# Performance work log

Measured on AMD Instinct MI355X. Metric: run time of the kernel, lower is better.

## Reference

```python
import jax, jax.numpy as jnp
import numpy as np

K = 12
CHUNK = 1024
N_LAYERS = 4
WIDTH = 192
COND = 64
PE_DIM = 3 * 8 * 2 + 3  # 51
OUT_SCALE = 0.01
BIG = 1e9


def _build_knn(x, k=K, chunk=CHUNK):
    """Brute-force kNN, row-chunked like the TF double-chunked version.
    x: (N,3) float32 -> (N,k) int32 neighbor indices (self excluded)."""
    n = x.shape[0]
    x = x.astype(jnp.float32)
    x_sq = jnp.sum(x * x, axis=1)  # (N,)
    col_ids = jnp.arange(n, dtype=jnp.int32)
    starts = jnp.arange(0, n, chunk, dtype=jnp.int32)

    def one_chunk(start):
        xc = jax.lax.dynamic_slice(x, (start, 0), (chunk, 3))        # (chunk,3)
        sq_c = jax.lax.dynamic_slice(x_sq, (start,), (chunk,))       # (chunk,)
        d = sq_c[:, None] + x_sq[None, :] - 2.0 * (xc @ x.T)         # (chunk,N)
        d = jnp.maximum(d, 0.0)
        rows = start + jnp.arange(chunk, dtype=jnp.int32)
        d = d + jnp.where(rows[:, None] == col_ids[None, :], BIG, 0.0)  # exclude self
        _, idx = jax.lax.top_k(-d, k)                                 # smallest distances
        return idx.astype(jnp.int32)

    idx = jax.lax.map(one_chunk, starts)  # (n/chunk, chunk, k)
    return idx.reshape(n, k)


def _fourier(x, Bs):
    """concat_k [sin(xB_k), cos(xB_k)] + x  -> (N, PE_DIM)."""
    feats = []
    for B in Bs:
        xb = x @ B  # (N,8)
        feats.append(jnp.sin(xb))
        feats.append(jnp.cos(xb))
    feats.append(x)
    return jnp.concatenate(feats, axis=-1)


def setup_inputs() -> dict:
    key = jax.random.key(0)
    ks = jax.random.split(key, 16)
    n = 32768
    x = jax.random.normal(ks[0], (n, 3), dtype=jnp.float32)
    z = jax.random.normal(ks[1], (COND,), dtype=jnp.float32)
    sigmas = (1.0, 10.0, 50.0)
    B0 = jax.random.normal(ks[2], (3, 8), dtype=jnp.float32) * sigmas[0]
    B1 = jax.random.normal(ks[3], (3, 8), dtype=jnp.float32) * sigmas[1]
    B2 = jax.random.normal(ks[4], (3, 8), dtype=jnp.float32) * sigmas[2]
    in_total = PE_DIM + COND  # 115
    s = 0.05
    Wp = jax.random.normal(ks[5], (in_total, WIDTH), dtype=jnp.float32) * s
    bp = jnp.zeros((WIDTH,), dtype=jnp.float32)
    mix_dim = WIDTH + WIDTH + 6  # feat + agg + rel_feat
    Wl = jax.random.normal(ks[6], (N_LAYERS, mix_dim, WIDTH), dtype=jnp.float32) * s
    bl = jnp.zeros((N_LAYERS, WIDTH), dtype=jnp.float32)
    # FiLM: kernel ~zeros, gamma bias=ones, beta bias=zeros (perturbed slightly)
    Wg = jax.random.normal(ks[7], (N_LAYERS, COND, WIDTH), dtype=jnp.float32) * 0.01
    bg = jnp.ones((N_LAYERS, WIDTH), dtype=jnp.float32)
    Wb = jax.random.normal(ks[8], (N_LAYERS, COND, WIDTH), dtype=jnp.float32) * 0.01
    bb = jnp.zeros((N_LAYERS, WIDTH), dtype=jnp.float32)
    Wout = jax.random.normal(ks[9], (WIDTH, 3), dtype=jnp.float32) * s
    bout = jnp.zeros((3,), dtype=jnp.float32)
    return {"x": x, "z": z, "B0": B0, "B1": B1, "B2": B2,
            "Wp": Wp, "bp": bp, "Wl": Wl, "bl": bl,
            "Wg": Wg, "bg": bg, "Wb": Wb, "bb": bb,
            "Wout": Wout, "bout": bout}


def reference(x, z, B0, B1, B2, Wp, bp, Wl, bl, Wg, bg, Wb, bb, Wout, bout):
    n = x.shape[0]
    knn_idx = _build_knn(x)                     # (N,K) int32
    pe = _fourier(x, (B0, B1, B2))              # (N,51)
    zb = jnp.broadcast_to(z[None, :], (n, COND))
    feat = jnp.concatenate([pe, zb], axis=-1)   # (N,115)
    h = jax.nn.silu(feat @ Wp + bp)             # (N,WIDTH)
    # precompute relative-coordinate stats (same for all layers)
    nbr_coords = x[knn_idx]                     # (N,K,3)
    rel = nbr_coords - x[:, None, :]
    rel_feat = jnp.concatenate([rel.mean(axis=1), rel.std(axis=1)], axis=-1)  # (N,6)
    for li in range(N_LAYERS):
        nbr = h[knn_idx]                        # (N,K,WIDTH) gather
        agg = nbr.mean(axis=1)                  # (N,WIDTH)
        mix = jnp.concatenate([h, agg, rel_feat], axis=-1)  # (N,390)
        h = jax.nn.silu(mix @ Wl[li] + bl[li])
        gamma = z @ Wg[li] + bg[li]             # (WIDTH,)
        beta = z @ Wb[li] + bb[li]
        h = h * gamma[None, :] + beta[None, :]  # FiLM
    out = (h @ Wout + bout) * OUT_SCALE         # (N,3)
    return out
```

## Files before the change

kernel.cpp:

```cpp
#include <hip/hip_runtime.h>
#include <math.h>

#define WIDTH 192
#define KNN 12
#define G 64
#define NCELLS (G * G * G)
#define SMAX 8

#define CE(a, b) { double _lo = fmin(a, b); double _hi = fmax(a, b); a = _lo; b = _hi; }
#define INSERT12(key) { \
    b11 = fmin(b11, key); \
    CE(b10, b11); CE(b9, b10); CE(b8, b9); CE(b7, b8); CE(b6, b7); \
    CE(b5, b6);  CE(b4, b5); CE(b3, b4); CE(b2, b3); CE(b1, b2); CE(b0, b1); }
#define DECL12 double b0,b1,b2,b3,b4,b5,b6,b7,b8,b9,b10,b11
#define INIT12 { b0=__hiloint2double(0x7F7FFFFF,0);  b1=__hiloint2double(0x7F7FFFFF,1); \
    b2=__hiloint2double(0x7F7FFFFF,2);  b3=__hiloint2double(0x7F7FFFFF,3); \
    b4=__hiloint2double(0x7F7FFFFF,4);  b5=__hiloint2double(0x7F7FFFFF,5); \
    b6=__hiloint2double(0x7F7FFFFF,6);  b7=__hiloint2double(0x7F7FFFFF,7); \
    b8=__hiloint2double(0x7F7FFFFF,8);  b9=__hiloint2double(0x7F7FFFFF,9); \
    b10=__hiloint2double(0x7F7FFFFF,10); b11=__hiloint2double(0x7F7FFFFF,11); }

#define MERGE_STAGE(m) { \
    double pb11 = shflx_d(b11, m), pb10 = shflx_d(b10, m), pb9 = shflx_d(b9, m); \
    double pb8  = shflx_d(b8, m),  pb7  = shflx_d(b7, m),  pb6 = shflx_d(b6, m); \
    double pb5  = shflx_d(b5, m),  pb4  = shflx_d(b4, m),  pb3 = shflx_d(b3, m); \
    double pb2  = shflx_d(b2, m),  pb1  = shflx_d(b1, m),  pb0 = shflx_d(b0, m); \
    double c12 = pb3, c13 = pb2, c14 = pb1, c15 = pb0; \
    b4 = fmin(b4, pb11); b5 = fmin(b5, pb10); b6 = fmin(b6, pb9);  b7 = fmin(b7, pb8); \
    b8 = fmin(b8, pb7);  b9 = fmin(b9, pb6);  b10 = fmin(b10, pb5); b11 = fmin(b11, pb4); \
    CE(b0, b8);  CE(b1, b9);  CE(b2, b10); CE(b3, b11); \
    CE(b4, c12); CE(b5, c13); CE(b6, c14); CE(b7, c15); \
    CE(b0, b4);  CE(b1, b5);  CE(b2, b6);  CE(b3, b7); \
    CE(b8, c12); CE(b9, c13); CE(b10, c14); CE(b11, c15); \
    CE(b0, b2);  CE(b1, b3);  CE(b4, b6);  CE(b5, b7); \
    CE(b8, b10); CE(b9, b11); \
    CE(b0, b1);  CE(b2, b3);  CE(b4, b5);  CE(b6, b7); \
    CE(b8, b9);  CE(b10, b11); }

__device__ inline unsigned encf(float f) {
    unsigned u = __float_as_uint(f);
    return (u & 0x80000000u) ? ~u : (u | 0x80000000u);
}
__device__ inline float decf(unsigned u) {
    return (u & 0x80000000u) ? __uint_as_float(u & 0x7fffffffu) : __uint_as_float(~u);
}
__device__ inline int cellc(float v, float mn, float invh) {
    int c = (int)((v - mn) * invh);
    return min(max(c, 0), G - 1);
}
__device__ inline double shflx_d(double v, int m) {
    int lo = __shfl_xor(__double2loint(v), m, 64);
    int hi = __shfl_xor(__double2hiint(v), m, 64);
    return __hiloint2double(hi, lo);
}

__global__ __launch_bounds__(256) void prep_kernel(
    const float4* __restrict__ sorted, const float* __restrict__ B0,
    const float* __restrict__ B1, const float* __restrict__ B2,
    float* __restrict__ pe, int n)
{
    int i = blockIdx.x * 256 + threadIdx.x;
    float4 q = sorted[i];
    float x0 = q.x, x1 = q.y, x2 = q.z;
    const float* Bm[3] = {B0, B1, B2};
    float* pr = pe + (size_t)i * 64;
#pragma unroll
    for (int m = 0; m < 3; ++m) {
        const float* B = Bm[m];
#pragma unroll
        for (int k = 0; k < 8; ++k) {
            float arg = x0 * B[k] + x1 * B[8 + k] + x2 * B[16 + k];
            pr[m * 16 + k]     = sinf(arg);
            pr[m * 16 + 8 + k] = cosf(arg);
        }
    }
    pr[48] = x0; pr[49] = x1; pr[50] = x2;
#pragma unroll
    for (int c = 51; c < 64; ++c) pr[c] = 0.0f;
}

__global__ __launch_bounds__(256) void precompute_kernel(
    const float* __restrict__ z, const float* __restrict__ Wp, const float* __restrict__ bp,
    const float* __restrict__ Wg, const float* __restrict__ bg,
    const float* __restrict__ Wb, const float* __restrict__ bb,
    float* __restrict__ bias0, float* __restrict__ gammaB, float* __restrict__ betaB)
{
    __shared__ float zs[64];
    int t = threadIdx.x;
    if (t < 64) zs[t] = z[t];
    __syncthreads();
    if (t < WIDTH) {
        float acc = bp[t];
        for (int k = 0; k < 64; ++k) acc += zs[k] * Wp[(51 + k) * WIDTH + t];
        bias0[t] = acc;
        for (int l = 0; l < 4; ++l) {
            float g = bg[l * WIDTH + t];
            float b = bb[l * WIDTH + t];
            for (int k = 0; k < 64; ++k) {
                g += zs[k] * Wg[(l * 64 + k) * WIDTH + t];
                b += zs[k] * Wb[(l * 64 + k) * WIDTH + t];
            }
            gammaB[l * WIDTH + t] = g;
            betaB[l * WIDTH + t] = b;
        }
    }
}

__global__ __launch_bounds__(64) void init_bbox_kernel(unsigned* __restrict__ bb)
{
    int t = threadIdx.x;
    if (t < 3) bb[t] = 0xFFFFFFFFu;
    else if (t < 6) bb[t] = 0u;
}

__global__ __launch_bounds__(256) void bbox_kernel(
    const float* __restrict__ x, unsigned* __restrict__ bb, int n)
{
    int i = blockIdx.x * 256 + threadIdx.x;
    unsigned emin[3], emax[3];
#pragma unroll
    for (int a = 0; a < 3; ++a) { unsigned e = encf(x[i * 3 + a]); emin[a] = e; emax[a] = e; }
#pragma unroll
    for (int o = 32; o; o >>= 1) {
#pragma unroll
        for (int a = 0; a < 3; ++a) {
            emin[a] = min(emin[a], (unsigned)__shfl_xor((int)emin[a], o, 64));
            emax[a] = max(emax[a], (unsigned)__shfl_xor((int)emax[a], o, 64));
        }
    }
    if ((threadIdx.x & 63) == 0) {
#pragma unroll
        for (int a = 0; a < 3; ++a) {
            atomicMin(&bb[a], emin[a]);
            atomicMax(&bb[3 + a], emax[a]);
        }
    }
}

__global__ __launch_bounds__(256) void hist_kernel(
    const float* __restrict__ x, const unsigned* __restrict__ bb,
    unsigned* __restrict__ counts, unsigned long long* __restrict__ rowmask, int n)
{
    int i = blockIdx.x * 256 + threadIdx.x;
    float mnx = decf(bb[0]), mny = decf(bb[1]), mnz = decf(bb[2]);
    float ivx = (float)G / (decf(bb[3]) - mnx);
    float ivy = (float)G / (decf(bb[4]) - mny);
    float ivz = (float)G / (decf(bb[5]) - mnz);
    int cx = cellc(x[i * 3 + 0], mnx, ivx);
    int cy = cellc(x[i * 3 + 1], mny, ivy);
    int cz = cellc(x[i * 3 + 2], mnz, ivz);
    atomicAdd(&counts[(cz * G + cy) * G + cx], 1u);
    atomicOr(&rowmask[cz * G + cy], 1ull << cx);
}

__global__ __launch_bounds__(256) void scan1_kernel(
    const unsigned* __restrict__ counts, unsigned* __restrict__ offs,
    unsigned* __restrict__ bsums)
{
    __shared__ unsigned s[256];
    int b = blockIdx.x, t = threadIdx.x;
    unsigned base = (unsigned)b * 1024 + t * 4;
    unsigned v[4], sum = 0;
#pragma unroll
    for (int k = 0; k < 4; ++k) { v[k] = counts[base + k]; sum += v[k]; }
    s[t] = sum; __syncthreads();
    for (int off = 1; off < 256; off <<= 1) {
        unsigned xv = (t >= off) ? s[t - off] : 0u;
        __syncthreads();
        s[t] += xv;
        __syncthreads();
    }
    unsigned excl = s[t] - sum;
    if (t == 255) bsums[b] = s[255];
    unsigned run = excl;
#pragma unroll
    for (int k = 0; k < 4; ++k) { offs[base + k] = run; run += v[k]; }
}

__global__ __launch_bounds__(256) void scan2_kernel(unsigned* __restrict__ bsums)
{
    __shared__ unsigned s[256];
    int t = threadIdx.x;
    unsigned v = bsums[t];
    s[t] = v; __syncthreads();
    for (int off = 1; off < 256; off <<= 1) {
        unsigned xv = (t >= off) ? s[t - off] : 0u;
        __syncthreads();
        s[t] += xv;
        __syncthreads();
    }
    bsums[t] = s[t] - v;
}

__global__ __launch_bounds__(256) void scan3_kernel(
    unsigned* __restrict__ offs, const unsigned* __restrict__ bsums,
    unsigned* __restrict__ cursors, int n)
{
    int b = blockIdx.x, t = threadIdx.x;
    unsigned add = bsums[b];
    unsigned base = (unsigned)b * 1024 + t * 4;
#pragma unroll
    for (int k = 0; k < 4; ++k) {
        unsigned v = offs[base + k] + add;
        offs[base + k] = v;
        cursors[base + k] = v;
    }
    if (b == 255 && t == 255) offs[NCELLS] = (unsigned)n;
}

__global__ __launch_bounds__(256) void scatter_kernel(
    const float* __restrict__ x, const unsigned* __restrict__ bb,
    unsigned* __restrict__ cursors, float4* __restrict__ sorted,
    unsigned* __restrict__ inv, int n)
{
    int i = blockIdx.x * 256 + threadIdx.x;
    float mnx = decf(bb[0]), mny = decf(bb[1]), mnz = decf(bb[2]);
    float ivx = (float)G / (decf(bb[3]) - mnx);
    float ivy = (float)G / (decf(bb[4]) - mny);
    float ivz = (float)G / (decf(bb[5]) - mnz);
    float x0 = x[i * 3 + 0], x1 = x[i * 3 + 1], x2 = x[i * 3 + 2];
    int cx = cellc(x0, mnx, ivx);
    int cy = cellc(x1, mny, ivy);
    int cz = cellc(x2, mnz, ivz);
    unsigned pos = atomicAdd(&cursors[(cz * G + cy) * G + cx], 1u);
    sorted[pos] = make_float4(x0, x1, x2, __int_as_float(i));
    inv[i] = pos;
}

__global__ __launch_bounds__(64) void knn_grid_kernel(
    const float4* __restrict__ sorted, const unsigned* __restrict__ offs,
    const unsigned long long* __restrict__ rowmask,
    const unsigned* __restrict__ bb, const float* __restrict__ x,
    const unsigned* __restrict__ inv,
    unsigned short* __restrict__ knn, float* __restrict__ relf, int n)
{
    const int l = threadIdx.x;
    const int l32 = l & 31;
    const int g32 = l >> 5;
    const int b = blockIdx.x;
    const int nch = n >> 6;
    const int ch = b >> 5, posb = b & 31;
    const int fch = (ch & 1) ? (nch - 1 - (ch >> 1)) : (ch >> 1);
    const int p = fch * 64 + posb * 2 + g32;

    float mnx = decf(bb[0]), mny = decf(bb[1]), mnz = decf(bb[2]);
    float mxx = decf(bb[3]), mxy = decf(bb[4]), mxz = decf(bb[5]);
    float hx = (mxx - mnx) / G, hy = (mxy - mny) / G, hz = (mxz - mnz) / G;
    float ivx = (float)G / (mxx - mnx);
    float ivy = (float)G / (mxy - mny);
    float ivz = (float)G / (mxz - mnz);

    float4 q = sorted[p];
    float xi = q.x, yi = q.y, zi = q.z;
    int iorig = __float_as_int(q.w);
    float sqi = fmaf(zi, zi, fmaf(yi, yi, xi * xi));
    int cx = cellc(xi, mnx, ivx), cy = cellc(yi, mny, ivy), cz = cellc(zi, mnz, ivz);
    float fx = (xi - mnx) - cx * hx;
    float fy = (yi - mny) - cy * hy;
    float fz = (zi - mnz) - cz * hz;

    DECL12; INIT12;
    float worst = 3.402823466e+38f;
    float worst_g = 3.402823466e+38f;
    int nc = 0;
    bool have12 = false;

    auto groupMinWorst = [&]() -> float {
        float wm = worst;
        wm = fminf(wm, __shfl_xor(wm, 1, 64));
        wm = fminf(wm, __shfl_xor(wm, 2, 64));
        wm = fminf(wm, __shfl_xor(wm, 4, 64));
        wm = fminf(wm, __shfl_xor(wm, 8, 64));
        wm = fminf(wm, __shfl_xor(wm, 16, 64));
        return wm;
    };

    auto lane12Bound = [&]() -> float {
        float v = __int_as_float(__double2hiint(b0));
#pragma unroll
        for (int k = 2; k <= 32; k <<= 1) {
#pragma unroll
            for (int j = k >> 1; j >= 1; j >>= 1) {
                float pv = __shfl_xor(v, j, 64);
                bool dir = ((l32 & k) == 0);
                bool lower = ((l32 & j) == 0);
                float mn = fminf(v, pv), mx = fmaxf(v, pv);
                v = (lower == dir) ? mn : mx;
            }
        }
        return __shfl(v, (l & 32) | 11, 64);
    };

    auto groupUnionD12 = [&]() -> float {
        double c0=b0,c1=b1,c2=b2,c3=b3,c4=b4,c5=b5,c6=b6,c7=b7,c8=b8,c9=b9,c10=b10,c11=b11;
        {
            double b0=c0,b1=c1,b2=c2,b3=c3,b4=c4,b5=c5,b6=c6,b7=c7,b8=c8,b9=c9,b10=c10,b11=c11;
#pragma unroll
            for (int m = 1; m <= 16; m <<= 1) MERGE_STAGE(m)
            return __int_as_float(__double2hiint(b11));
        }
    };

    auto scanRange = [&](int c0, int c1) {
        unsigned j0 = offs[c0], j1 = offs[c1 + 1];
        if (j0 >= j1) return;
        float4 c = sorted[j0];
        for (unsigned t = j0; t < j1; ++t) {
            unsigned tn = (t + 1 < j1) ? t + 1 : t;
            float4 nx = sorted[tn];
            float sqj = fmaf(c.z, c.z, fmaf(c.y, c.y, c.x * c.x));
            float dot = fmaf(zi, c.z, fmaf(yi, c.y, xi * c.x));
            float d = fmaf(-2.0f, dot, sqi + sqj);
            int jg = __float_as_int(c.w);
            if (d <= fminf(worst, worst_g) && jg != iorig) {
                d = fmaxf(d, 0.0f);
                double key = __hiloint2double(__float_as_int(d), jg);
                INSERT12(key);
                worst = __int_as_float(__double2hiint(b11));
                ++nc;
            }
            c = nx;
        }
    };

    auto scanStrided = [&](int c0, int c1, int sub, int step) {
        unsigned j0 = offs[c0], j1 = offs[c1 + 1];
        for (unsigned t = j0 + sub; t < j1; t += step) {
            float4 c = sorted[t];
            float sqj = fmaf(c.z, c.z, fmaf(c.y, c.y, c.x * c.x));
            float dot = fmaf(zi, c.z, fmaf(yi, c.y, xi * c.x));
            float d = fmaf(-2.0f, dot, sqi + sqj);
            int jg = __float_as_int(c.w);
            if (d <= fminf(worst, worst_g) && jg != iorig) {
                d = fmaxf(d, 0.0f);
                double key = __hiloint2double(__float_as_int(d), jg);
                INSERT12(key);
                worst = __int_as_float(__double2hiint(b11));
                ++nc;
            }
        }
    };

    auto doRow = [&](int s, int dz, int dy, int sub, int step) {
        int zz = cz + dz, yy = cy + dy;
        if (zz < 0 || zz >= G || yy < 0 || yy >= G) return;
        int row = zz * G + yy;
        unsigned long long rm = rowmask[row];
        if (rm == 0ull) return;
        int rb = row * G;
        int adz = dz < 0 ? -dz : dz, ady = dy < 0 ? -dy : dy;
        if (adz == s || ady == s) {
            int x0 = max(cx - s, 0), x1 = min(cx + s, G - 1);
            unsigned long long msk =
                ((x1 == 63) ? ~0ull : ((1ull << (x1 + 1)) - 1ull)) &
                ~((1ull << x0) - 1ull);
            unsigned long long mm = rm & msk;
            if (mm) {
                int c0 = __ffsll((unsigned long long)mm) - 1;
                int c1 = 63 - __clzll((long long)mm);
                if (step == 1) scanRange(rb + c0, rb + c1);
                else           scanStrided(rb + c0, rb + c1, sub, step);
            }
        } else {
            int xm = cx - s, xp = cx + s;
            if (xm >= 0 && ((rm >> xm) & 1ull)) {
                if (step == 1) scanRange(rb + xm, rb + xm);
                else           scanStrided(rb + xm, rb + xm, sub, step);
            }
            if (xp < G && ((rm >> xp) & 1ull)) {
                if (step == 1) scanRange(rb + xp, rb + xp);
                else           scanStrided(rb + xp, rb + xp, sub, step);
            }
        }
    };

    auto check12 = [&]() {
        if (!have12) {
            int ns = nc;
#pragma unroll
            for (int o = 1; o <= 16; o <<= 1) ns += __shfl_xor(ns, o, 64);
            have12 = (ns >= 12);
        }
    };

    bool done = false;
    for (int s = 0; s <= SMAX; ++s) {
        if (s > 0) {
            float bx = (s - 1) * hx + fminf(fx, hx - fx);
            float by = (s - 1) * hy + fminf(fy, hy - fy);
            float bz = (s - 1) * hz + fminf(fz, hz - fz);
            float bnd = fminf(bx, fminf(by, bz));
            float bnd2 = bnd * bnd;
            worst_g = fminf(worst_g, groupMinWorst());
            if (bnd2 > worst_g + 1e-4f) { done = true; break; }
            unsigned long long anyb =
                __ballot(__double2hiint(b0) != 0x7F7FFFFF);
            unsigned gm = (unsigned)(anyb >> (g32 << 5));
            if (__popc(gm) >= 12) {
                worst_g = fminf(worst_g, lane12Bound());
                if (bnd2 > worst_g + 1e-4f) { done = true; break; }
            }
            if (s >= 2) {
                check12();
                if (have12) {
                    worst_g = fminf(worst_g, groupUnionD12());
                    if (bnd2 > worst_g + 1e-4f) { done = true; break; }
                }
            }
        }
        if (s == 0) {
            int row = cz * G + cy;
            if ((rowmask[row] >> cx) & 1ull) {
                int rb = row * G;
                scanStrided(rb + cx, rb + cx, l32, 32);
            }
        } else {
            int w2 = 2 * s + 1;
            int nrows = w2 * w2;
            int lpr = 32 / nrows;
            if (lpr > 1) {
                int r = l32 / lpr, sub = l32 - r * lpr;
                if (r < nrows) {
                    int dz = r / w2 - s, dy = r - (r / w2) * w2 - s;
                    doRow(s, dz, dy, sub, lpr);
                }
            } else {
                float rcp = 1.0f / (float)w2;
                for (int r = l32; r < nrows; r += 32) {
                    int qd = (int)((float)r * rcp);
                    int rem = r - qd * w2;
                    if (rem < 0) { qd--; rem += w2; }
                    else if (rem >= w2) { qd++; rem -= w2; }
                    doRow(s, qd - s, rem - s, 0, 1);
                }
            }
        }
    }
    if (!done) {
        float bx = SMAX * hx + fminf(fx, hx - fx);
        float by = SMAX * hy + fminf(fy, hy - fy);
        float bz = SMAX * hz + fminf(fz, hz - fz);
        float bnd = fminf(bx, fminf(by, bz));
        float bnd2 = bnd * bnd;
        worst_g = fminf(worst_g, groupMinWorst());
        if (bnd2 > worst_g + 1e-4f) done = true;
        if (!done) {
            unsigned long long anyb =
                __ballot(__double2hiint(b0) != 0x7F7FFFFF);
            unsigned gm = (unsigned)(anyb >> (g32 << 5));
            if (__popc(gm) >= 12) {
                worst_g = fminf(worst_g, lane12Bound());
                if (bnd2 > worst_g + 1e-4f) done = true;
            }
        }
        if (!done) {
            check12();
            if (have12) {
                worst_g = fminf(worst_g, groupUnionD12());
                if (bnd2 > worst_g + 1e-4f) done = true;
            }
        }
    }
    if (!done) {
        INIT12;
        worst = 3.402823466e+38f;
        for (int base = 0; base < n; base += 256) {
            float4 cc[8];
#pragma unroll
            for (int r = 0; r < 8; ++r) cc[r] = sorted[base + l32 + r * 32];
#pragma unroll
            for (int r = 0; r < 8; ++r) {
                float4 c = cc[r];
                float sqj = fmaf(c.z, c.z, fmaf(c.y, c.y, c.x * c.x));
                float dot = fmaf(zi, c.z, fmaf(yi, c.y, xi * c.x));
                float d = fmaf(-2.0f, dot, sqi + sqj);
                int jg = __float_as_int(c.w);
                if (d <= fminf(worst, worst_g) && jg != iorig) {
                    d = fmaxf(d, 0.0f);
                    double key = __hiloint2double(__float_as_int(d), jg);
                    INSERT12(key);
                    worst = __int_as_float(__double2hiint(b11));
                }
            }
        }
    }

#pragma unroll
    for (int m = 1; m <= 16; m <<= 1) MERGE_STAGE(m)

    if (l32 == 0) {
        int idx[KNN];
        idx[0]=__double2loint(b0);  idx[1]=__double2loint(b1);  idx[2]=__double2loint(b2);
        idx[3]=__double2loint(b3);  idx[4]=__double2loint(b4);  idx[5]=__double2loint(b5);
        idx[6]=__double2loint(b6);  idx[7]=__double2loint(b7);  idx[8]=__double2loint(b8);
        idx[9]=__double2loint(b9);  idx[10]=__double2loint(b10); idx[11]=__double2loint(b11);

        float rx[KNN], ry[KNN], rz[KNN];
        float sx = 0.f, sy = 0.f, sz = 0.f;
#pragma unroll
        for (int s = 0; s < KNN; ++s) {
            int j = idx[s];
            knn[(size_t)p * KNN + s] = (unsigned short)inv[j];
            rx[s] = x[(size_t)j * 3 + 0] - xi;
            ry[s] = x[(size_t)j * 3 + 1] - yi;
            rz[s] = x[(size_t)j * 3 + 2] - zi;
            sx += rx[s]; sy += ry[s]; sz += rz[s];
        }
        float mx = sx / 12.0f, my = sy / 12.0f, mz = sz / 12.0f;
        float vx = 0.f, vy = 0.f, vz = 0.f;
#pragma unroll
        for (int s = 0; s < KNN; ++s) {
            float dx = rx[s] - mx, dy = ry[s] - my, dz = rz[s] - mz;
            vx += dx * dx; vy += dy * dy; vz += dz * dz;
        }
        float* rr = relf + (size_t)p * 8;
        rr[0] = mx; rr[1] = my; rr[2] = mz;
        rr[3] = sqrtf(vx / 12.0f); rr[4] = sqrtf(vy / 12.0f); rr[5] = sqrtf(vz / 12.0f);
        rr[6] = 0.0f; rr[7] = 0.0f;
    }
}

template <bool LAYER>
__global__ __launch_bounds__(256) void gemm_silu_kernel(
    const float* __restrict__ A0, const unsigned short* __restrict__ knnp,
    const float* __restrict__ Rel,
    const float* __restrict__ W, const float* __restrict__ bias,
    const float* __restrict__ gamma, const float* __restrict__ beta,
    float* __restrict__ out)
{
    __shared__ float As[16][68];
    __shared__ float Bs[16][196];
    const int tid = threadIdx.x;
    const int ty = tid >> 4, tx = tid & 15;
    const int m0 = blockIdx.x * 64;
    const int arow = tid >> 2, akoff = (tid & 3) * 4;
    const int bk = tid >> 4,  bc = (tid & 15) * 12;

    float acc[4][12] = {};
    const int NCH = LAYER ? 24 : 4;

    unsigned kf[6] = {0, 0, 0, 0, 0, 0};
    if (LAYER) {
        const unsigned* kp = (const unsigned*)(knnp + (size_t)(m0 + arow) * KNN);
#pragma unroll
        for (int w = 0; w < 6; ++w) kf[w] = kp[w];
    }

    auto loadA = [&](int ch) -> float4 {
        int k0 = ch * 16;
        if (!LAYER) {
            return *(const float4*)&A0[(size_t)(m0 + arow) * 64 + k0 + akoff];
        } else if (k0 < 192) {
            return *(const float4*)&A0[(size_t)(m0 + arow) * 192 + k0 + akoff];
        } else {
            int c4 = (k0 - 192 + akoff) >> 2;
            const float4* h4 = (const float4*)A0;
            float4 s = make_float4(0.f, 0.f, 0.f, 0.f);
#pragma unroll
            for (int j = 0; j < KNN; ++j) {
                unsigned idx = (j & 1) ? (kf[j >> 1] >> 16) : (kf[j >> 1] & 0xFFFFu);
                float4 v = h4[(size_t)idx * 48 + c4];
                s.x += v.x; s.y += v.y; s.z += v.z; s.w += v.w;
            }
            const float r = 1.0f / 12.0f;
            return make_float4(s.x * r, s.y * r, s.z * r, s.w * r);
        }
    };

    float4 ra = loadA(0);
    const float* wr0 = &W[(size_t)bk * 192 + bc];
    float4 rb0 = *(const float4*)&wr0[0];
    float4 rb1 = *(const float4*)&wr0[4];
    float4 rb2 = *(const float4*)&wr0[8];

    for (int ch = 0; ch < NCH; ++ch) {
        As[akoff + 0][arow] = ra.x; As[akoff + 1][arow] = ra.y;
        As[akoff + 2][arow] = ra.z; As[akoff + 3][arow] = ra.w;
        *(float4*)&Bs[bk][bc + 0] = rb0;
        *(float4*)&Bs[bk][bc + 4] = rb1;
        *(float4*)&Bs[bk][bc + 8] = rb2;
        __syncthreads();
        if (ch + 1 < NCH) {
            ra = loadA(ch + 1);
            const float* wr = &W[(size_t)((ch + 1) * 16 + bk) * 192 + bc];
            rb0 = *(const float4*)&wr[0];
            rb1 = *(const float4*)&wr[4];
            rb2 = *(const float4*)&wr[8];
        }
#pragma unroll
        for (int k = 0; k < 16; ++k) {
            float4 a0 = *(const float4*)&As[k][ty * 4];
            float av[4] = {a0.x, a0.y, a0.z, a0.w};
            float4 q0 = *(const float4*)&Bs[k][tx * 12 + 0];
            float4 q1 = *(const float4*)&Bs[k][tx * 12 + 4];
            float4 q2 = *(const float4*)&Bs[k][tx * 12 + 8];
            float bv[12] = {q0.x, q0.y, q0.z, q0.w, q1.x, q1.y, q1.z, q1.w,
                            q2.x, q2.y, q2.z, q2.w};
#pragma unroll
            for (int a = 0; a < 4; ++a)
#pragma unroll
                for (int bcol = 0; bcol < 12; ++bcol)
                    acc[a][bcol] = fmaf(av[a], bv[bcol], acc[a][bcol]);
        }
        __syncthreads();
    }

    if (LAYER) {
        {
            int row = tid >> 2, cp = (tid & 3) * 2;
            float2 v = *(const float2*)&Rel[(size_t)(m0 + row) * 8 + cp];
            As[cp + 0][row] = v.x; As[cp + 1][row] = v.y;
        }
        {
            int k2 = tid >> 4, c = (tid & 15) * 12;
            if (k2 < 8) {
                int gk = 384 + k2; if (gk > 389) gk = 389;
                const float* wr = &W[(size_t)gk * 192 + c];
                *(float4*)&Bs[k2][c + 0] = *(const float4*)&wr[0];
                *(float4*)&Bs[k2][c + 4] = *(const float4*)&wr[4];
                *(float4*)&Bs[k2][c + 8] = *(const float4*)&wr[8];
            }
        }
        __syncthreads();
#pragma unroll
        for (int k = 0; k < 8; ++k) {
            float4 a0 = *(const float4*)&As[k][ty * 4];
            float av[4] = {a0.x, a0.y, a0.z, a0.w};
            float4 q0 = *(const float4*)&Bs[k][tx * 12 + 0];
            float4 q1 = *(const float4*)&Bs[k][tx * 12 + 4];
            float4 q2 = *(const float4*)&Bs[k][tx * 12 + 8];
            float bv[12] = {q0.x, q0.y, q0.z, q0.w, q1.x, q1.y, q1.z, q1.w,
                            q2.x, q2.y, q2.z, q2.w};
#pragma unroll
            for (int a = 0; a < 4; ++a)
#pragma unroll
                for (int bcol = 0; bcol < 12; ++bcol)
                    acc[a][bcol] = fmaf(av[a], bv[bcol], acc[a][bcol]);
        }
        __syncthreads();
    }

#pragma unroll
    for (int a = 0; a < 4; ++a) {
        int gi = m0 + ty * 4 + a;
        float res[12];
#pragma unroll
        for (int bcol = 0; bcol < 12; ++bcol) {
            int gc = tx * 12 + bcol;
            float v = acc[a][bcol] + bias[gc];
            float s = 1.0f / (1.0f + expf(-v));
            v = v * s;
            if (LAYER) v = v * gamma[gc] + beta[gc];
            res[bcol] = v;
        }
        float* orow = &out[(size_t)gi * 192 + tx * 12];
        *(float4*)&orow[0] = make_float4(res[0], res[1], res[2], res[3]);
        *(float4*)&orow[4] = make_float4(res[4], res[5], res[6], res[7]);
        *(float4*)&orow[8] = make_float4(res[8], res[9], res[10], res[11]);
    }
}

__global__ __launch_bounds__(256) void out_kernel(
    const float4* __restrict__ h4, const float4* __restrict__ sorted,
    const float* __restrict__ Wout, const float* __restrict__ bout,
    float* __restrict__ out, int n)
{
    __shared__ float w[576];
    int t = threadIdx.x;
    for (int e = t; e < 576; e += 256) w[e] = Wout[e];
    __syncthreads();
    int i = blockIdx.x * 256 + t;
    float a0 = 0.f, a1 = 0.f, a2 = 0.f;
    for (int k4 = 0; k4 < 48; ++k4) {
        float4 hv = h4[(size_t)i * 48 + k4];
        int k = k4 * 4;
        a0 = fmaf(hv.x, w[k * 3 + 0], a0); a1 = fmaf(hv.x, w[k * 3 + 1], a1); a2 = fmaf(hv.x, w[k * 3 + 2], a2);
        a0 = fmaf(hv.y, w[k * 3 + 3], a0); a1 = fmaf(hv.y, w[k * 3 + 4], a1); a2 = fmaf(hv.y, w[k * 3 + 5], a2);
        a0 = fmaf(hv.z, w[k * 3 + 6], a0); a1 = fmaf(hv.z, w[k * 3 + 7], a1); a2 = fmaf(hv.z, w[k * 3 + 8], a2);
        a0 = fmaf(hv.w, w[k * 3 + 9], a0); a1 = fmaf(hv.w, w[k * 3 + 10], a1); a2 = fmaf(hv.w, w[k * 3 + 11], a2);
    }
    int iorig = __float_as_int(sorted[i].w);
    out[(size_t)iorig * 3 + 0] = (a0 + bout[0]) * 0.01f;
    out[(size_t)iorig * 3 + 1] = (a1 + bout[1]) * 0.01f;
    out[(size_t)iorig * 3 + 2] = (a2 + bout[2]) * 0.01f;
}

extern "C" void kernel_launch(void* const* d_in, const int* in_sizes, int n_in,
                              void* d_out, int out_size, void* d_ws, size_t ws_size,
                              hipStream_t stream)
{
    const float* x    = (const float*)d_in[0];
    const float* z    = (const float*)d_in[1];
    const float* B0   = (const float*)d_in[2];
    const float* B1   = (const float*)d_in[3];
    const float* B2   = (const float*)d_in[4];
    const float* Wp   = (const float*)d_in[5];
    const float* bp   = (const float*)d_in[6];
    const float* Wl   = (const float*)d_in[7];
    const float* bl   = (const float*)d_in[8];
    const float* Wg   = (const float*)d_in[9];
    const float* bg   = (const float*)d_in[10];
    const float* Wb   = (const float*)d_in[11];
    const float* bb   = (const float*)d_in[12];
    const float* Wout = (const float*)d_in[13];
    const float* bout = (const float*)d_in[14];

    int n = in_sizes[0] / 3;

    float* ws = (float*)d_ws;
    float* bias0  = ws;
    float* gammaB = ws + 192;
    float* betaB  = ws + 960;
    size_t off = 1728;
    unsigned short* knn = (unsigned short*)(ws + off);  off += (size_t)n * 6;
    float* relf = ws + off;                off += (size_t)n * 8;
    float4* sorted = (float4*)(ws + off);  off += (size_t)n * 4;
    float* hA   = ws + off;                off += (size_t)n * 192;
    float* hB   = ws + off;                off += (size_t)n * 192;

    unsigned* bbx     = (unsigned*)hA;
    unsigned* counts  = bbx + 8;
    unsigned* offsA   = counts + NCELLS;
    unsigned* cursors = offsA + NCELLS + 1;
    unsigned* bsums   = cursors + NCELLS;
    size_t gu = 8 + (size_t)NCELLS * 3 + 1 + 256;
    gu = (gu + 1) & ~(size_t)1;
    unsigned long long* rowmask = (unsigned long long*)((unsigned*)hA + gu);
    gu += (size_t)G * G * 2;
    unsigned* inv = (unsigned*)hA + gu;
    float* pe = hB;

    init_bbox_kernel<<<1, 64, 0, stream>>>(bbx);
    hipMemsetAsync(counts, 0, (size_t)NCELLS * 4, stream);
    hipMemsetAsync(rowmask, 0, (size_t)G * G * 8, stream);
    precompute_kernel<<<1, 256, 0, stream>>>(z, Wp, bp, Wg, bg, Wb, bb,
                                             bias0, gammaB, betaB);
    bbox_kernel<<<n / 256, 256, 0, stream>>>(x, bbx, n);
    hist_kernel<<<n / 256, 256, 0, stream>>>(x, bbx, counts, rowmask, n);
    scan1_kernel<<<NCELLS / 1024, 256, 0, stream>>>(counts, offsA, bsums);
    scan2_kernel<<<1, 256, 0, stream>>>(bsums);
    scan3_kernel<<<NCELLS / 1024, 256, 0, stream>>>(offsA, bsums, cursors, n);
    scatter_kernel<<<n / 256, 256, 0, stream>>>(x, bbx, cursors, sorted, inv, n);
    prep_kernel<<<n / 256, 256, 0, stream>>>(sorted, B0, B1, B2, pe, n);
    knn_grid_kernel<<<n / 2, 64, 0, stream>>>(sorted, offsA, rowmask, bbx, x,
                                              inv, knn, relf, n);

    gemm_silu_kernel<false><<<n / 64, 256, 0, stream>>>(
        pe, nullptr, nullptr, Wp, bias0, nullptr, nullptr, hA);

    float* hcur = hA;
    float* hnxt = hB;
    for (int li = 0; li < 4; ++li) {
        gemm_silu_kernel<true><<<n / 64, 256, 0, stream>>>(
            hcur, knn, relf,
            Wl + (size_t)li * 390 * 192, bl + (size_t)li * 192,
            gammaB + (size_t)li * 192, betaB + (size_t)li * 192, hnxt);
        float* t = hcur; hcur = hnxt; hnxt = t;
    }

    out_kernel<<<n / 256, 256, 0, stream>>>((const float4*)hcur, sorted,
                                            Wout, bout, (float*)d_out, n);
}
```

Before: 740.0 us.

## Schedule kNN chunks by density-based cost ordering instead of alternating ends

The scatter pass now records each point's cell occupancy count. A new kernel takes the minimum count per 64-point chunk, and another bitonic-sorts the chunks by that key. The kNN kernel then processes chunks in this order, so sparse chunks, whose searches likely expand wider and run longer, are dispatched first. This replaces the previous alternating front/back chunk schedule and is meant to reduce tail imbalance, at the cost of two small extra kernel launches and extra memory traffic.

```diff
diff --git a/kernel.cpp b/kernel.cpp
--- a/kernel.cpp
+++ b/kernel.cpp
@@ -210,8 +210,9 @@
 
 __global__ __launch_bounds__(256) void scatter_kernel(
     const float* __restrict__ x, const unsigned* __restrict__ bb,
+    const unsigned* __restrict__ counts,
     unsigned* __restrict__ cursors, float4* __restrict__ sorted,
-    unsigned* __restrict__ inv, int n)
+    unsigned* __restrict__ inv, unsigned* __restrict__ keyq, int n)
 {
     int i = blockIdx.x * 256 + threadIdx.x;
     float mnx = decf(bb[0]), mny = decf(bb[1]), mnz = decf(bb[2]);
@@ -222,26 +223,58 @@
     int cx = cellc(x0, mnx, ivx);
     int cy = cellc(x1, mny, ivy);
     int cz = cellc(x2, mnz, ivz);
-    unsigned pos = atomicAdd(&cursors[(cz * G + cy) * G + cx], 1u);
+    int cell = (cz * G + cy) * G + cx;
+    unsigned pos = atomicAdd(&cursors[cell], 1u);
     sorted[pos] = make_float4(x0, x1, x2, __int_as_float(i));
     inv[i] = pos;
+    keyq[pos] = counts[cell];
+}
+
+__global__ __launch_bounds__(64) void chunkmin_kernel(
+    const unsigned* __restrict__ keyq, unsigned* __restrict__ ckey)
+{
+    int t = threadIdx.x;
+    unsigned v = keyq[blockIdx.x * 64 + t];
+#pragma unroll
+    for (int o = 32; o; o >>= 1)
+        v = min(v, (unsigned)__shfl_xor((int)v, o, 64));
+    if (t == 0) ckey[blockIdx.x] = v;
+}
+
+__global__ __launch_bounds__(512) void chunksort_kernel(
+    const unsigned* __restrict__ ckey, unsigned short* __restrict__ corder, int nch)
+{
+    __shared__ unsigned s[512];
+    int t = threadIdx.x;
+    s[t] = (t < nch) ? ((min(ckey[t], 0xFFFFu) << 16) | (unsigned)t) : 0xFFFFFFFFu;
+    __syncthreads();
+    for (int k = 2; k <= 512; k <<= 1) {
+        for (int j = k >> 1; j >= 1; j >>= 1) {
+            int ixj = t ^ j;
+            if (ixj > t) {
+                unsigned a = s[t], c = s[ixj];
+                bool asc = ((t & k) == 0);
+                if ((a > c) == asc) { s[t] = c; s[ixj] = a; }
+            }
+            __syncthreads();
+        }
+    }
+    if (t < nch) corder[t] = (unsigned short)(s[t] & 0xFFFFu);
 }
 
 __global__ __launch_bounds__(64) void knn_grid_kernel(
     const float4* __restrict__ sorted, const unsigned* __restrict__ offs,
     const unsigned long long* __restrict__ rowmask,
     const unsigned* __restrict__ bb, const float* __restrict__ x,
-    const unsigned* __restrict__ inv,
+    const unsigned* __restrict__ inv, const unsigned short* __restrict__ corder,
     unsigned short* __restrict__ knn, float* __restrict__ relf, int n)
 {
     const int l = threadIdx.x;
     const int l32 = l & 31;
     const int g32 = l >> 5;
     const int b = blockIdx.x;
-    const int nch = n >> 6;
-    const int ch = b >> 5, posb = b & 31;
-    const int fch = (ch & 1) ? (nch - 1 - (ch >> 1)) : (ch >> 1);
-    const int p = fch * 64 + posb * 2 + g32;
+    const int chk = corder[b >> 5];
+    const int p = chk * 64 + (b & 31) * 2 + g32;
 
     float mnx = decf(bb[0]), mny = decf(bb[1]), mnz = decf(bb[2]);
     float mxx = decf(bb[3]), mxy = decf(bb[4]), mxz = decf(bb[5]);
@@ -728,7 +761,12 @@
     unsigned long long* rowmask = (unsigned long long*)((unsigned*)hA + gu);
     gu += (size_t)G * G * 2;
     unsigned* inv = (unsigned*)hA + gu;
+    unsigned* keyq = inv + n;
+    unsigned* ckey = keyq + n;
+    unsigned short* corder = (unsigned short*)(ckey + 512);
     float* pe = hB;
+
+    int nch = n >> 6;
 
     init_bbox_kernel<<<1, 64, 0, stream>>>(bbx);
     hipMemsetAsync(counts, 0, (size_t)NCELLS * 4, stream);
@@ -740,10 +778,13 @@
     scan1_kernel<<<NCELLS / 1024, 256, 0, stream>>>(counts, offsA, bsums);
     scan2_kernel<<<1, 256, 0, stream>>>(bsums);
     scan3_kernel<<<NCELLS / 1024, 256, 0, stream>>>(offsA, bsums, cursors, n);
-    scatter_kernel<<<n / 256, 256, 0, stream>>>(x, bbx, cursors, sorted, inv, n);
+    scatter_kernel<<<n / 256, 256, 0, stream>>>(x, bbx, counts, cursors,
+                                                sorted, inv, keyq, n);
+    chunkmin_kernel<<<nch, 64, 0, stream>>>(keyq, ckey);
+    chunksort_kernel<<<1, 512, 0, stream>>>(ckey, corder, nch);
     prep_kernel<<<n / 256, 256, 0, stream>>>(sorted, B0, B1, B2, pe, n);
     knn_grid_kernel<<<n / 2, 64, 0, stream>>>(sorted, offsA, rowmask, bbx, x,
-                                              inv, knn, relf, n);
+                                              inv, corder, knn, relf, n);
 
     gemm_silu_kernel<false><<<n / 64, 256, 0, stream>>>(
         pe, nullptr, nullptr, Wp, bias0, nullptr, nullptr, hA);
```

Result: slower. 759.7 us (+2.7%).

## Fuse Fourier features, output projection and scan/init into neighboring kernels

Applied to the files above, without the earlier changes.

The Fourier-feature prep kernel is removed and sin/cos features are computed on the fly in the first GEMM's A-tile loader. The final output projection is folded into the last layer GEMM epilogue, which reduces across lanes with shuffles, so the last hidden state is never written or re-read. The scan2 kernel is dropped (each scan3 block reduces the earlier block sums itself), and the two memsets plus the bbox init become one init kernel. Fewer launches and less global traffic, in exchange for transcendental work repeated per tile and redundant block-sum reductions.

```diff
diff --git a/kernel.cpp b/kernel.cpp
--- a/kernel.cpp
+++ b/kernel.cpp
@@ -54,31 +54,6 @@
     return __hiloint2double(hi, lo);
 }
 
-__global__ __launch_bounds__(256) void prep_kernel(
-    const float4* __restrict__ sorted, const float* __restrict__ B0,
-    const float* __restrict__ B1, const float* __restrict__ B2,
-    float* __restrict__ pe, int n)
-{
-    int i = blockIdx.x * 256 + threadIdx.x;
-    float4 q = sorted[i];
-    float x0 = q.x, x1 = q.y, x2 = q.z;
-    const float* Bm[3] = {B0, B1, B2};
-    float* pr = pe + (size_t)i * 64;
-#pragma unroll
-    for (int m = 0; m < 3; ++m) {
-        const float* B = Bm[m];
-#pragma unroll
-        for (int k = 0; k < 8; ++k) {
-            float arg = x0 * B[k] + x1 * B[8 + k] + x2 * B[16 + k];
-            pr[m * 16 + k]     = sinf(arg);
-            pr[m * 16 + 8 + k] = cosf(arg);
-        }
-    }
-    pr[48] = x0; pr[49] = x1; pr[50] = x2;
-#pragma unroll
-    for (int c = 51; c < 64; ++c) pr[c] = 0.0f;
-}
-
 __global__ __launch_bounds__(256) void precompute_kernel(
     const float* __restrict__ z, const float* __restrict__ Wp, const float* __restrict__ bp,
     const float* __restrict__ Wg, const float* __restrict__ bg,
@@ -106,11 +81,15 @@
     }
 }
 
-__global__ __launch_bounds__(64) void init_bbox_kernel(unsigned* __restrict__ bb)
-{
-    int t = threadIdx.x;
-    if (t < 3) bb[t] = 0xFFFFFFFFu;
-    else if (t < 6) bb[t] = 0u;
+__global__ __launch_bounds__(256) void init_kernel(
+    unsigned* __restrict__ bb, unsigned* __restrict__ counts,
+    unsigned long long* __restrict__ rowmask)
+{
+    int i = blockIdx.x * 256 + threadIdx.x;
+    if (i < 3) bb[i] = 0xFFFFFFFFu;
+    else if (i < 6) bb[i] = 0u;
+    counts[i] = 0u;
+    if (i < G * G) rowmask[i] = 0ull;
 }
 
 __global__ __launch_bounds__(256) void bbox_kernel(
@@ -177,27 +156,19 @@
     for (int k = 0; k < 4; ++k) { offs[base + k] = run; run += v[k]; }
 }
 
-__global__ __launch_bounds__(256) void scan2_kernel(unsigned* __restrict__ bsums)
-{
-    __shared__ unsigned s[256];
-    int t = threadIdx.x;
-    unsigned v = bsums[t];
-    s[t] = v; __syncthreads();
-    for (int off = 1; off < 256; off <<= 1) {
-        unsigned xv = (t >= off) ? s[t - off] : 0u;
-        __syncthreads();
-        s[t] += xv;
-        __syncthreads();
-    }
-    bsums[t] = s[t] - v;
-}
-
 __global__ __launch_bounds__(256) void scan3_kernel(
     unsigned* __restrict__ offs, const unsigned* __restrict__ bsums,
     unsigned* __restrict__ cursors, int n)
 {
+    __shared__ unsigned s[256];
     int b = blockIdx.x, t = threadIdx.x;
-    unsigned add = bsums[b];
+    s[t] = (t < b) ? bsums[t] : 0u;
+    __syncthreads();
+    for (int off = 128; off; off >>= 1) {
+        if (t < off) s[t] += s[t + off];
+        __syncthreads();
+    }
+    unsigned add = s[0];
     unsigned base = (unsigned)b * 1024 + t * 4;
 #pragma unroll
     for (int k = 0; k < 4; ++k) {
@@ -520,16 +491,20 @@
     }
 }
 
-template <bool LAYER>
+template <int MODE>
 __global__ __launch_bounds__(256) void gemm_silu_kernel(
     const float* __restrict__ A0, const unsigned short* __restrict__ knnp,
-    const float* __restrict__ Rel,
+    const float* __restrict__ Rel, const float4* __restrict__ sorted4,
+    const float* __restrict__ Bf0, const float* __restrict__ Bf1,
+    const float* __restrict__ Bf2,
     const float* __restrict__ W, const float* __restrict__ bias,
     const float* __restrict__ gamma, const float* __restrict__ beta,
-    float* __restrict__ out)
+    const float* __restrict__ Wout, const float* __restrict__ bout,
+    float* __restrict__ hout, float* __restrict__ fout)
 {
     __shared__ float As[16][68];
     __shared__ float Bs[16][196];
+    __shared__ float wouts[576];
     const int tid = threadIdx.x;
     const int ty = tid >> 4, tx = tid & 15;
     const int m0 = blockIdx.x * 64;
@@ -537,10 +512,20 @@
     const int bk = tid >> 4,  bc = (tid & 15) * 12;
 
     float acc[4][12] = {};
-    const int NCH = LAYER ? 24 : 4;
+    const int NCH = (MODE == 0) ? 4 : 24;
+
+    if (MODE == 2) {
+        for (int e = tid; e < 576; e += 256) wouts[e] = Wout[e];
+    }
+
+    float qx = 0.f, qy = 0.f, qz = 0.f;
+    if (MODE == 0) {
+        float4 qq = sorted4[m0 + arow];
+        qx = qq.x; qy = qq.y; qz = qq.z;
+    }
 
     unsigned kf[6] = {0, 0, 0, 0, 0, 0};
-    if (LAYER) {
+    if (MODE != 0) {
         const unsigned* kp = (const unsigned*)(knnp + (size_t)(m0 + arow) * KNN);
 #pragma unroll
         for (int w = 0; w < 6; ++w) kf[w] = kp[w];
@@ -548,8 +533,28 @@
 
     auto loadA = [&](int ch) -> float4 {
         int k0 = ch * 16;
-        if (!LAYER) {
-            return *(const float4*)&A0[(size_t)(m0 + arow) * 64 + k0 + akoff];
+        if (MODE == 0) {
+            int c0 = k0 + akoff;
+            float v[4];
+            if (c0 < 48) {
+                int m = c0 >> 4, jb = c0 & 15;
+                const float* B = (m == 0) ? Bf0 : (m == 1) ? Bf1 : Bf2;
+                bool iscos = jb >= 8;
+                int j0 = iscos ? jb - 8 : jb;
+#pragma unroll
+                for (int e = 0; e < 4; ++e) {
+                    int j = j0 + e;
+                    float arg = qx * B[j] + qy * B[8 + j] + qz * B[16 + j];
+                    v[e] = iscos ? cosf(arg) : sinf(arg);
+                }
+            } else {
+#pragma unroll
+                for (int e = 0; e < 4; ++e) {
+                    int c = c0 + e;
+                    v[e] = (c == 48) ? qx : (c == 49) ? qy : (c == 50) ? qz : 0.0f;
+                }
+            }
+            return make_float4(v[0], v[1], v[2], v[3]);
         } else if (k0 < 192) {
             return *(const float4*)&A0[(size_t)(m0 + arow) * 192 + k0 + akoff];
         } else {
@@ -605,7 +610,7 @@
         __syncthreads();
     }
 
-    if (LAYER) {
+    if (MODE != 0) {
         {
             int row = tid >> 2, cp = (tid & 3) * 2;
             float2 v = *(const float2*)&Rel[(size_t)(m0 + row) * 8 + cp];
@@ -640,6 +645,7 @@
         __syncthreads();
     }
 
+    float po[4][3] = {};
 #pragma unroll
     for (int a = 0; a < 4; ++a) {
         int gi = m0 + ty * 4 + a;
@@ -650,39 +656,48 @@
             float v = acc[a][bcol] + bias[gc];
             float s = 1.0f / (1.0f + expf(-v));
             v = v * s;
-            if (LAYER) v = v * gamma[gc] + beta[gc];
+            if (MODE != 0) v = v * gamma[gc] + beta[gc];
             res[bcol] = v;
         }
-        float* orow = &out[(size_t)gi * 192 + tx * 12];
-        *(float4*)&orow[0] = make_float4(res[0], res[1], res[2], res[3]);
-        *(float4*)&orow[4] = make_float4(res[4], res[5], res[6], res[7]);
-        *(float4*)&orow[8] = make_float4(res[8], res[9], res[10], res[11]);
-    }
-}
-
-__global__ __launch_bounds__(256) void out_kernel(
-    const float4* __restrict__ h4, const float4* __restrict__ sorted,
-    const float* __restrict__ Wout, const float* __restrict__ bout,
-    float* __restrict__ out, int n)
-{
-    __shared__ float w[576];
-    int t = threadIdx.x;
-    for (int e = t; e < 576; e += 256) w[e] = Wout[e];
-    __syncthreads();
-    int i = blockIdx.x * 256 + t;
-    float a0 = 0.f, a1 = 0.f, a2 = 0.f;
-    for (int k4 = 0; k4 < 48; ++k4) {
-        float4 hv = h4[(size_t)i * 48 + k4];
-        int k = k4 * 4;
-        a0 = fmaf(hv.x, w[k * 3 + 0], a0); a1 = fmaf(hv.x, w[k * 3 + 1], a1); a2 = fmaf(hv.x, w[k * 3 + 2], a2);
-        a0 = fmaf(hv.y, w[k * 3 + 3], a0); a1 = fmaf(hv.y, w[k * 3 + 4], a1); a2 = fmaf(hv.y, w[k * 3 + 5], a2);
-        a0 = fmaf(hv.z, w[k * 3 + 6], a0); a1 = fmaf(hv.z, w[k * 3 + 7], a1); a2 = fmaf(hv.z, w[k * 3 + 8], a2);
-        a0 = fmaf(hv.w, w[k * 3 + 9], a0); a1 = fmaf(hv.w, w[k * 3 + 10], a1); a2 = fmaf(hv.w, w[k * 3 + 11], a2);
-    }
-    int iorig = __float_as_int(sorted[i].w);
-    out[(size_t)iorig * 3 + 0] = (a0 + bout[0]) * 0.01f;
-    out[(size_t)iorig * 3 + 1] = (a1 + bout[1]) * 0.01f;
-    out[(size_t)iorig * 3 + 2] = (a2 + bout[2]) * 0.01f;
+        if (MODE == 2) {
+#pragma unroll
+            for (int e = 0; e < 12; ++e) {
+                int c = tx * 12 + e;
+                po[a][0] = fmaf(res[e], wouts[c * 3 + 0], po[a][0]);
+                po[a][1] = fmaf(res[e], wouts[c * 3 + 1], po[a][1]);
+                po[a][2] = fmaf(res[e], wouts[c * 3 + 2], po[a][2]);
+            }
+        } else {
+            float* orow = &hout[(size_t)gi * 192 + tx * 12];
+            *(float4*)&orow[0] = make_float4(res[0], res[1], res[2], res[3]);
+            *(float4*)&orow[4] = make_float4(res[4], res[5], res[6], res[7]);
+            *(float4*)&orow[8] = make_float4(res[8], res[9], res[10], res[11]);
+        }
+    }
+
+    if (MODE == 2) {
+#pragma unroll
+        for (int a = 0; a < 4; ++a)
+#pragma unroll
+            for (int j = 0; j < 3; ++j) {
+                float v = po[a][j];
+                v += __shfl_xor(v, 1, 64);
+                v += __shfl_xor(v, 2, 64);
+                v += __shfl_xor(v, 4, 64);
+                v += __shfl_xor(v, 8, 64);
+                po[a][j] = v;
+            }
+        if (tx == 0) {
+#pragma unroll
+            for (int a = 0; a < 4; ++a) {
+                int gi = m0 + ty * 4 + a;
+                int iorig = __float_as_int(sorted4[gi].w);
+                fout[(size_t)iorig * 3 + 0] = (po[a][0] + bout[0]) * 0.01f;
+                fout[(size_t)iorig * 3 + 1] = (po[a][1] + bout[1]) * 0.01f;
+                fout[(size_t)iorig * 3 + 2] = (po[a][2] + bout[2]) * 0.01f;
+            }
+        }
+    }
 }
 
 extern "C" void kernel_launch(void* const* d_in, const int* in_sizes, int n_in,
@@ -728,36 +743,35 @@
     unsigned long long* rowmask = (unsigned long long*)((unsigned*)hA + gu);
     gu += (size_t)G * G * 2;
     unsigned* inv = (unsigned*)hA + gu;
-    float* pe = hB;
-
-    init_bbox_kernel<<<1, 64, 0, stream>>>(bbx);
-    hipMemsetAsync(counts, 0, (size_t)NCELLS * 4, stream);
-    hipMemsetAsync(rowmask, 0, (size_t)G * G * 8, stream);
+
+    init_kernel<<<NCELLS / 256, 256, 0, stream>>>(bbx, counts, rowmask);
     precompute_kernel<<<1, 256, 0, stream>>>(z, Wp, bp, Wg, bg, Wb, bb,
                                              bias0, gammaB, betaB);
     bbox_kernel<<<n / 256, 256, 0, stream>>>(x, bbx, n);
     hist_kernel<<<n / 256, 256, 0, stream>>>(x, bbx, counts, rowmask, n);
     scan1_kernel<<<NCELLS / 1024, 256, 0, stream>>>(counts, offsA, bsums);
-    scan2_kernel<<<1, 256, 0, stream>>>(bsums);
     scan3_kernel<<<NCELLS / 1024, 256, 0, stream>>>(offsA, bsums, cursors, n);
     scatter_kernel<<<n / 256, 256, 0, stream>>>(x, bbx, cursors, sorted, inv, n);
-    prep_kernel<<<n / 256, 256, 0, stream>>>(sorted, B0, B1, B2, pe, n);
     knn_grid_kernel<<<n / 2, 64, 0, stream>>>(sorted, offsA, rowmask, bbx, x,
                                               inv, knn, relf, n);
 
-    gemm_silu_kernel<false><<<n / 64, 256, 0, stream>>>(
-        pe, nullptr, nullptr, Wp, bias0, nullptr, nullptr, hA);
+    gemm_silu_kernel<0><<<n / 64, 256, 0, stream>>>(
+        nullptr, nullptr, nullptr, sorted, B0, B1, B2,
+        Wp, bias0, nullptr, nullptr, nullptr, nullptr, hA, nullptr);
 
     float* hcur = hA;
     float* hnxt = hB;
-    for (int li = 0; li < 4; ++li) {
-        gemm_silu_kernel<true><<<n / 64, 256, 0, stream>>>(
-            hcur, knn, relf,
+    for (int li = 0; li < 3; ++li) {
+        gemm_silu_kernel<1><<<n / 64, 256, 0, stream>>>(
+            hcur, knn, relf, nullptr, nullptr, nullptr, nullptr,
             Wl + (size_t)li * 390 * 192, bl + (size_t)li * 192,
-            gammaB + (size_t)li * 192, betaB + (size_t)li * 192, hnxt);
+            gammaB + (size_t)li * 192, betaB + (size_t)li * 192,
+            nullptr, nullptr, hnxt, nullptr);
         float* t = hcur; hcur = hnxt; hnxt = t;
     }
-
-    out_kernel<<<n / 256, 256, 0, stream>>>((const float4*)hcur, sorted,
-                                            Wout, bout, (float*)d_out, n);
-}
+    gemm_silu_kernel<2><<<n / 64, 256, 0, stream>>>(
+        hcur, knn, relf, sorted, nullptr, nullptr, nullptr,
+        Wl + (size_t)3 * 390 * 192, bl + (size_t)3 * 192,
+        gammaB + (size_t)3 * 192, betaB + (size_t)3 * 192,
+        Wout, bout, nullptr, (float*)d_out);
+}
```

Measured after the change: 682.5 us. 7.8% less time.
